# Kernel optimization log

Measured on AMD Instinct MI355X. Metric: run time of the kernel, lower is better.

The kernel has to match this reference:

```python
import jax, jax.numpy as jnp
import numpy as np

N_EMBED = 2048
N_HEAD = 16
HEAD_SIZE = N_EMBED // N_HEAD  # 128


def rotate_half(x):
    x1, x2 = jnp.split(x, 2, axis=-1)
    return jnp.concatenate((-x2, x1), axis=-1)


def setup_inputs() -> dict:
    key = jax.random.key(0)
    k_x, k_qkv, k_proj, k_b = jax.random.split(key, 4)
    B, T = 4, 2048
    x = jax.random.normal(k_x, (B, T, N_EMBED), dtype=jnp.float32)
    # weights stored as [in, out] so y = x @ W (equivalent param'n of nn.Linear)
    w_qkv = jax.random.normal(k_qkv, (N_EMBED, 3 * N_EMBED), dtype=jnp.float32) * (N_EMBED ** -0.5)
    w_proj = jax.random.normal(k_proj, (N_EMBED, N_EMBED), dtype=jnp.float32) * (N_EMBED ** -0.5)
    b_proj = jax.random.normal(k_b, (N_EMBED,), dtype=jnp.float32) * 0.02
    return {"x": x, "w_qkv": w_qkv, "w_proj": w_proj, "b_proj": b_proj}


def reference(x, w_qkv, w_proj, b_proj):
    B, T, C = x.shape
    H, D = N_HEAD, HEAD_SIZE
    qkv = x @ w_qkv                                   # [B,T,3C]
    q, k, v = jnp.split(qkv, 3, axis=2)
    q = q.reshape(B, T, H, D).transpose(0, 2, 1, 3)   # [B,H,T,D]
    k = k.reshape(B, T, H, D).transpose(0, 2, 1, 3)
    v = v.reshape(B, T, H, D).transpose(0, 2, 1, 3)
    # RoPE in fp32
    inv_freq = 1.0 / (10000.0 ** (jnp.arange(0, D, 2, dtype=jnp.float32) / D))
    t = jnp.arange(T, dtype=jnp.float32)
    freqs = jnp.einsum('i,j->ij', t, inv_freq)        # [T,D/2]
    emb = jnp.concatenate((freqs, freqs), axis=-1)    # [T,D]
    cos = jnp.cos(emb)[None, None, :, :]
    sin = jnp.sin(emb)[None, None, :, :]
    qf = q.astype(jnp.float32)
    kf = k.astype(jnp.float32)
    q = (qf * cos + rotate_half(qf) * sin).astype(v.dtype)
    k = (kf * cos + rotate_half(kf) * sin).astype(v.dtype)
    # causal SDPA
    scale = 1.0 / jnp.sqrt(jnp.asarray(D, dtype=q.dtype))
    scores = jnp.einsum('bhqd,bhkd->bhqk', q, k) * scale
    causal = jnp.tril(jnp.ones((T, T), dtype=bool))
    scores = jnp.where(causal[None, None, :, :], scores, jnp.finfo(scores.dtype).min)
    attn = jax.nn.softmax(scores, axis=-1)
    out = jnp.einsum('bhqk,bhkd->bhqd', attn, v)      # [B,H,T,D]
    out = out.transpose(0, 2, 1, 3).reshape(B, T, C)
    return out @ w_proj + b_proj
```

## Files before the change

kernel.cpp:

```cpp
#include <hip/hip_runtime.h>
#include <hip/hip_bf16.h>
#include <cstdint>
#include <cstddef>

typedef __bf16 bf16x8 __attribute__((ext_vector_type(8)));
typedef __bf16 bf16x4 __attribute__((ext_vector_type(4)));
typedef float  f32x4  __attribute__((ext_vector_type(4)));

__device__ __forceinline__ void lds_load16(const void* gsrc, void* ldst) {
    __builtin_amdgcn_global_load_lds(
        (const __attribute__((address_space(1))) unsigned int*)gsrc,
        (__attribute__((address_space(3))) unsigned int*)ldst,
        16, 0, 0);
}

__global__ __launch_bounds__(256) void cvt_k(const float* __restrict__ in,
                                             __bf16* __restrict__ out, int n8) {
    int i = blockIdx.x * 256 + threadIdx.x;
    if (i >= n8) return;
    const float4* p4 = (const float4*)in + (size_t)i * 2;
    float4 a = p4[0], b = p4[1];
    bf16x8 o;
    o[0] = (__bf16)a.x; o[1] = (__bf16)a.y; o[2] = (__bf16)a.z; o[3] = (__bf16)a.w;
    o[4] = (__bf16)b.x; o[5] = (__bf16)b.y; o[6] = (__bf16)b.z; o[7] = (__bf16)b.w;
    *((bf16x8*)out + i) = o;
}

__global__ __launch_bounds__(256) void transp_k(const float* __restrict__ W,
                                                __bf16* __restrict__ WT, int R, int C) {
    __shared__ float tile[32][33];
    int tx = threadIdx.x & 31, ty = threadIdx.x >> 5;
    int c0 = blockIdx.x * 32, r0 = blockIdx.y * 32;
#pragma unroll
    for (int k = 0; k < 4; ++k)
        tile[ty + 8 * k][tx] = W[(size_t)(r0 + ty + 8 * k) * C + c0 + tx];
    __syncthreads();
#pragma unroll
    for (int k = 0; k < 4; ++k)
        WT[(size_t)(c0 + ty + 8 * k) * R + r0 + tx] = (__bf16)tile[tx][ty + 8 * k];
}

__global__ __launch_bounds__(256) void sincos_k(float2* __restrict__ sc) {
    int idx = blockIdx.x * 256 + threadIdx.x;
    int t = idx >> 6, j = idx & 63;
    float inv = powf(10000.f, -(float)j / 64.f);
    float f = (float)t * inv;
    float s, c;
    sincosf(f, &s, &c);
    sc[idx] = make_float2(c, s);
}

__global__ __launch_bounds__(512, 2) void gemm8_k(const __bf16* __restrict__ A,
                                                  const __bf16* __restrict__ Bt,
                                                  int nbn, int mode,
                                                  __bf16* __restrict__ qb, __bf16* __restrict__ kb,
                                                  __bf16* __restrict__ vt,
                                                  float* __restrict__ outp,
                                                  const float* __restrict__ bias,
                                                  const float2* __restrict__ sc) {
    __shared__ __bf16 lds[2][2][2][128 * 64];
    const int K = 2048, NT = K / 64;
    int nwg = gridDim.x;
    int per = nwg >> 3;
    int bid = blockIdx.x;
    int wg = (bid & 7) * per + (bid >> 3);
    int bm = wg / nbn, bn = wg % nbn;
    int m0 = bm * 256, n0 = bn * 256;
    int tid = threadIdx.x;
    int lane = tid & 63, wave = tid >> 6;
    int wm = wave >> 2, wn = wave & 3;
    int lr = lane & 15, lg = lane >> 4;

    f32x4 acc[8][4] = {};

    auto stageA = [&](int db, int sub, int kt) {
#pragma unroll
        for (int l = 0; l < 2; ++l) {
            int chunk = l * 512 + tid;
            int r = chunk >> 3, c16 = chunk & 7;
            int rg = m0 + ((r >> 6) << 7) + (sub << 6) + (r & 63);
            lds_load16(A + (size_t)rg * K + (kt << 6) + ((c16 ^ (r & 7)) << 3),
                       &lds[db][0][sub][chunk * 8]);
        }
    };
    auto stageB = [&](int db, int sub, int kt) {
#pragma unroll
        for (int l = 0; l < 2; ++l) {
            int chunk = l * 512 + tid;
            int r = chunk >> 3, c16 = chunk & 7;
            int rg = n0 + ((r >> 5) << 6) + (sub << 5) + (r & 31);
            lds_load16(Bt + (size_t)rg * K + (kt << 6) + ((c16 ^ (r & 7)) << 3),
                       &lds[db][1][sub][chunk * 8]);
        }
    };
    auto rdA = [&](int db, int sub, int q, int kk) -> bf16x8 {
        int r = (wm << 6) + (q << 4) + lr;
        int cb = ((kk << 6) + (lg << 4)) ^ ((r & 7) << 4);
        return *(const bf16x8*)((const char*)&lds[db][0][sub][0] + r * 128 + cb);
    };
    auto rdB = [&](int db, int j, int kk) -> bf16x8 {
        int sub = j >> 1;
        int r = (wn << 5) + ((j & 1) << 4) + lr;
        int cb = ((kk << 6) + (lg << 4)) ^ ((r & 7) << 4);
        return *(const bf16x8*)((const char*)&lds[db][1][sub][0] + r * 128 + cb);
    };

    stageA(0, 0, 0); stageB(0, 0, 0); stageB(0, 1, 0); stageA(0, 1, 0);
    stageA(1, 0, 1); stageB(1, 0, 1);
    asm volatile("s_waitcnt vmcnt(8)" ::: "memory");
    __builtin_amdgcn_s_barrier();

    bf16x8 a[4][2], bA[2][2], bB[2][2];
    for (int t = 0; t < NT; ++t) {
        int db = t & 1, dn = db ^ 1;
        bool pf1 = (t + 1 < NT), pf2 = (t + 2 < NT);
#pragma unroll
        for (int q = 0; q < 4; ++q) { a[q][0] = rdA(db, 0, q, 0); a[q][1] = rdA(db, 0, q, 1); }
#pragma unroll
        for (int j = 0; j < 2; ++j) { bA[j][0] = rdB(db, j, 0); bA[j][1] = rdB(db, j, 1); }
        if (pf1) stageB(dn, 1, t + 1);
        __builtin_amdgcn_s_barrier();
        asm volatile("s_waitcnt lgkmcnt(0)" ::: "memory");
        __builtin_amdgcn_sched_barrier(0);
        __builtin_amdgcn_s_setprio(1);
#pragma unroll
        for (int q = 0; q < 4; ++q)
#pragma unroll
            for (int j = 0; j < 2; ++j)
#pragma unroll
                for (int kk = 0; kk < 2; ++kk)
                    acc[q][j] = __builtin_amdgcn_mfma_f32_16x16x32_bf16(a[q][kk], bA[j][kk], acc[q][j], 0, 0, 0);
        __builtin_amdgcn_s_setprio(0);
        if (pf2) asm volatile("s_waitcnt vmcnt(6)" ::: "memory");
        else     asm volatile("s_waitcnt vmcnt(0)" ::: "memory");
        __builtin_amdgcn_s_barrier();
#pragma unroll
        for (int j = 0; j < 2; ++j) { bB[j][0] = rdB(db, j + 2, 0); bB[j][1] = rdB(db, j + 2, 1); }
        if (pf1) stageA(dn, 1, t + 1);
        __builtin_amdgcn_s_barrier();
        asm volatile("s_waitcnt lgkmcnt(0)" ::: "memory");
        __builtin_amdgcn_sched_barrier(0);
        __builtin_amdgcn_s_setprio(1);
#pragma unroll
        for (int q = 0; q < 4; ++q)
#pragma unroll
            for (int j = 0; j < 2; ++j)
#pragma unroll
                for (int kk = 0; kk < 2; ++kk)
                    acc[q][j + 2] = __builtin_amdgcn_mfma_f32_16x16x32_bf16(a[q][kk], bB[j][kk], acc[q][j + 2], 0, 0, 0);
        __builtin_amdgcn_s_setprio(0);
        __builtin_amdgcn_s_barrier();
#pragma unroll
        for (int q = 0; q < 4; ++q) { a[q][0] = rdA(db, 1, q, 0); a[q][1] = rdA(db, 1, q, 1); }
        if (pf2) stageA(db, 0, t + 2);
        __builtin_amdgcn_s_barrier();
        asm volatile("s_waitcnt lgkmcnt(0)" ::: "memory");
        __builtin_amdgcn_sched_barrier(0);
        __builtin_amdgcn_s_setprio(1);
#pragma unroll
        for (int q = 0; q < 4; ++q)
#pragma unroll
            for (int j = 0; j < 2; ++j)
#pragma unroll
                for (int kk = 0; kk < 2; ++kk)
                    acc[q + 4][j + 2] = __builtin_amdgcn_mfma_f32_16x16x32_bf16(a[q][kk], bB[j][kk], acc[q + 4][j + 2], 0, 0, 0);
        __builtin_amdgcn_s_setprio(0);
        __builtin_amdgcn_s_barrier();
        if (pf2) stageB(db, 0, t + 2);
        __builtin_amdgcn_s_setprio(1);
#pragma unroll
        for (int q = 0; q < 4; ++q)
#pragma unroll
            for (int j = 0; j < 2; ++j)
#pragma unroll
                for (int kk = 0; kk < 2; ++kk)
                    acc[q + 4][j] = __builtin_amdgcn_mfma_f32_16x16x32_bf16(a[q][kk], bA[j][kk], acc[q + 4][j], 0, 0, 0);
        __builtin_amdgcn_s_setprio(0);
        if (pf2)      asm volatile("s_waitcnt vmcnt(8)" ::: "memory");
        else if (pf1) asm volatile("s_waitcnt vmcnt(4)" ::: "memory");
        __builtin_amdgcn_s_barrier();
    }

    if (mode == 0) {
        int which = n0 >> 11;
        if (which == 2) {
#pragma unroll
            for (int q = 0; q < 8; ++q) {
                int row_t = (wm << 7) + ((q >> 2) << 6) + ((q & 3) << 4) + (lg << 2);
#pragma unroll
                for (int j = 0; j < 4; ++j) {
                    int c = n0 + (wn << 6) + (j << 4) + lr;
                    int h = (c & 2047) >> 7, d = c & 127;
#pragma unroll
                    for (int r = 0; r < 4; ++r) {
                        int row = m0 + row_t + r;
                        int b_ = row >> 11, tt = row & 2047;
                        vt[((size_t)(b_ * 16 + h) * 128 + d) * 2048 + tt] = (__bf16)acc[q][j][r];
                    }
                }
            }
        } else {
            __bf16* dst = (which == 0) ? qb : kb;
            float scale = (which == 0) ? 0.08838834764831845f : 1.f;
            int rl = (wm << 4) + (lg << 2);
            int colw = (wn << 6);
#pragma unroll
            for (int q = 0; q < 8; ++q) {
                float* scr = (float*)&lds[q & 1][0][0][0];
                int row_t = (wm << 7) + ((q >> 2) << 6) + ((q & 3) << 4) + (lg << 2);
#pragma unroll
                for (int j = 0; j < 4; ++j)
#pragma unroll
                    for (int r = 0; r < 4; ++r)
                        scr[(rl + r) * 260 + colw + (j << 4) + lr] = acc[q][j][r];
                __syncthreads();
#pragma unroll
                for (int j = 0; j < 4; ++j) {
                    int c = n0 + colw + (j << 4) + lr;
                    int h = (c & 2047) >> 7, d = c & 127;
                    int jj = (j << 4) + lr;
#pragma unroll
                    for (int r = 0; r < 4; ++r) {
                        int row = m0 + row_t + r;
                        int b_ = row >> 11, tt = row & 2047;
                        float2 cs = sc[tt * 64 + jj];
                        float v0 = acc[q][j][r];
                        float v1 = scr[(rl + r) * 260 + (colw ^ 64) + (j << 4) + lr];
                        float o = ((wn & 1) == 0) ? (v0 * cs.x - v1 * cs.y)
                                                  : (v0 * cs.x + v1 * cs.y);
                        dst[((size_t)(b_ * 16 + h) * 2048 + tt) * 128 + d] = (__bf16)(o * scale);
                    }
                }
            }
        }
    } else {
#pragma unroll
        for (int q = 0; q < 8; ++q) {
            int row_t = (wm << 7) + ((q >> 2) << 6) + ((q & 3) << 4) + (lg << 2);
#pragma unroll
            for (int j = 0; j < 4; ++j) {
                int col = n0 + (wn << 6) + (j << 4) + lr;
                float bv = bias[col];
#pragma unroll
                for (int r = 0; r < 4; ++r) {
                    int row = m0 + row_t + r;
                    outp[(size_t)row * 2048 + col] = acc[q][j][r] + bv;
                }
            }
        }
    }
}

__global__ __launch_bounds__(512, 2) void attn_k(const __bf16* __restrict__ qb,
                                                 const __bf16* __restrict__ kb,
                                                 const __bf16* __restrict__ vt,
                                                 __bf16* __restrict__ ao) {
    __shared__ __bf16 Ks[64 * 128];
    __shared__ __bf16 Vs[128 * 64];
    __shared__ __bf16 Ps[8][16 * 64];

    int bid = blockIdx.x;
    int qt = 15 - (bid >> 6);
    int bh = bid & 63;
    int qs = qt * 128;
    int tid = threadIdx.x, wave = tid >> 6, lane = tid & 63;
    int lr = lane & 15, lg = lane >> 4;

    bf16x8 qf[4];
    const __bf16* Qrow = qb + ((size_t)bh * 2048 + qs + wave * 16 + lr) * 128;
#pragma unroll
    for (int kk = 0; kk < 4; ++kk) qf[kk] = *(const bf16x8*)(Qrow + kk * 32 + lg * 8);

    f32x4 ot[8] = {};
    float m_run = -1e30f, l_run = 0.f;
    int qmax = qs + wave * 16 + 15;
    int kend = qs + 64;

    for (int ks = 0; ks <= kend; ks += 64) {
#pragma unroll
        for (int i = 0; i < 2; ++i) {
            int c = tid + i * 512;
            {
                int row = c >> 4;
                int cc = c ^ (row & 7);
                int dd = (cc & 15) * 8;
                lds_load16(kb + ((size_t)bh * 2048 + ks + row) * 128 + dd, Ks + c * 8);
            }
            {
                int row = c >> 3;
                int cc = c ^ (row & 7);
                int tt = (cc & 7) * 8;
                lds_load16(vt + ((size_t)bh * 128 + row) * 2048 + ks + tt, Vs + c * 8);
            }
        }
        __syncthreads();

        if (ks <= qmax) {
            f32x4 st[4];
            __builtin_amdgcn_s_setprio(1);
#pragma unroll
            for (int mt = 0; mt < 4; ++mt) {
                f32x4 s = {};
#pragma unroll
                for (int kk = 0; kk < 4; ++kk) {
                    int row = mt * 16 + lr;
                    const __bf16* kp = Ks + row * 128 + ((((kk * 64 + lg * 16)) ^ ((row & 7) << 4)) >> 1);
                    bf16x8 afr = *(const bf16x8*)kp;
                    s = __builtin_amdgcn_mfma_f32_16x16x32_bf16(afr, qf[kk], s, 0, 0, 0);
                }
                st[mt] = s;
            }
            __builtin_amdgcn_s_setprio(0);

            if (ks + 63 > qs + wave * 16) {
                int q = qs + wave * 16 + lr;
#pragma unroll
                for (int mt = 0; mt < 4; ++mt)
#pragma unroll
                    for (int r = 0; r < 4; ++r) {
                        int kv = ks + mt * 16 + lg * 4 + r;
                        if (kv > q) st[mt][r] = -1e30f;
                    }
            }

            float pm = -1e30f;
#pragma unroll
            for (int mt = 0; mt < 4; ++mt)
#pragma unroll
                for (int r = 0; r < 4; ++r) pm = fmaxf(pm, st[mt][r]);
            pm = fmaxf(pm, __shfl_xor(pm, 16));
            pm = fmaxf(pm, __shfl_xor(pm, 32));
            float nm = fmaxf(m_run, pm);
            float alpha = __expf(m_run - nm);
            float psum = 0.f;
#pragma unroll
            for (int mt = 0; mt < 4; ++mt)
#pragma unroll
                for (int r = 0; r < 4; ++r) {
                    float p = __expf(st[mt][r] - nm);
                    psum += p;
                    st[mt][r] = p;
                }
            psum += __shfl_xor(psum, 16);
            psum += __shfl_xor(psum, 32);
            l_run = l_run * alpha + psum;
            m_run = nm;
#pragma unroll
            for (int t8 = 0; t8 < 8; ++t8) ot[t8] *= alpha;

#pragma unroll
            for (int mt = 0; mt < 4; ++mt) {
                bf16x4 pk;
#pragma unroll
                for (int r = 0; r < 4; ++r) pk[r] = (__bf16)st[mt][r];
                int byteoff = lr * 128 + (((mt * 32 + lg * 8)) ^ ((lr & 7) << 4));
                *(bf16x4*)((char*)&Ps[wave][0] + byteoff) = pk;
            }

            bf16x8 pfr[2];
#pragma unroll
            for (int kk = 0; kk < 2; ++kk) {
                const char* pp = (const char*)&Ps[wave][0] + lr * 128 + (((kk * 64 + lg * 16)) ^ ((lr & 7) << 4));
                pfr[kk] = *(const bf16x8*)pp;
            }
            __builtin_amdgcn_s_setprio(1);
#pragma unroll
            for (int dt = 0; dt < 8; ++dt) {
#pragma unroll
                for (int kk = 0; kk < 2; ++kk) {
                    int row = dt * 16 + lr;
                    const __bf16* vp = Vs + row * 64 + ((((kk * 64 + lg * 16)) ^ ((row & 7) << 4)) >> 1);
                    bf16x8 afr = *(const bf16x8*)vp;
                    ot[dt] = __builtin_amdgcn_mfma_f32_16x16x32_bf16(afr, pfr[kk], ot[dt], 0, 0, 0);
                }
            }
            __builtin_amdgcn_s_setprio(0);
        }
        __syncthreads();
    }

    float inv = 1.f / l_run;
    int b_ = bh >> 4, h = bh & 15;
    size_t rowbase = ((size_t)b_ * 2048 + qs + wave * 16 + lr) * 2048 + h * 128;
#pragma unroll
    for (int dt = 0; dt < 8; ++dt) {
        bf16x4 o;
#pragma unroll
        for (int r = 0; r < 4; ++r) o[r] = (__bf16)(ot[dt][r] * inv);
        *(bf16x4*)(ao + rowbase + dt * 16 + lg * 4) = o;
    }
}

extern "C" void kernel_launch(void* const* d_in, const int* in_sizes, int n_in,
                              void* d_out, int out_size, void* d_ws, size_t ws_size,
                              hipStream_t stream) {
    const float* x      = (const float*)d_in[0];
    const float* w_qkv  = (const float*)d_in[1];
    const float* w_proj = (const float*)d_in[2];
    const float* b_proj = (const float*)d_in[3];
    float* out = (float*)d_out;
    char* ws = (char*)d_ws;

    __bf16* xb  = (__bf16*)(ws);
    __bf16* wqt = (__bf16*)(ws + 33554432);
    __bf16* wpt = (__bf16*)(ws + 58720256);
    __bf16* qb  = (__bf16*)(ws + 67108864);
    __bf16* kb  = (__bf16*)(ws + 100663296);
    __bf16* vt  = (__bf16*)(ws + 134217728);
    __bf16* ao  = (__bf16*)(ws + 167772160);
    float2* sc  = (float2*)(ws + 201326592);

    hipLaunchKernelGGL(cvt_k, dim3(8192), dim3(256), 0, stream, x, xb, 2097152);
    hipLaunchKernelGGL(transp_k, dim3(192, 64), dim3(256), 0, stream, w_qkv, wqt, 2048, 6144);
    hipLaunchKernelGGL(transp_k, dim3(64, 64), dim3(256), 0, stream, w_proj, wpt, 2048, 2048);
    hipLaunchKernelGGL(sincos_k, dim3(512), dim3(256), 0, stream, sc);
    hipLaunchKernelGGL(gemm8_k, dim3(768), dim3(512), 0, stream,
                       xb, wqt, 24, 0, qb, kb, vt, (float*)nullptr, (const float*)nullptr, sc);
    hipLaunchKernelGGL(attn_k, dim3(1024), dim3(512), 0, stream, qb, kb, vt, ao);
    hipLaunchKernelGGL(gemm8_k, dim3(256), dim3(512), 0, stream,
                       ao, wpt, 8, 1, (__bf16*)nullptr, (__bf16*)nullptr, (__bf16*)nullptr,
                       out, b_proj, (const float2*)nullptr);
}
```

Before: 394.8 us.

## Merge prep kernels into one launch and add lazy softmax rescaling

The four preprocessing kernels (x conversion, two weight transposes, sincos table) become a single launch whose blocks branch on block index, cutting launch overhead and inter-kernel gaps. Separately, the attention online softmax now skips the max update and output rescaling whenever the new tile max stays within 8 of the running max across the wavefront. That avoids one exp and the eight output multiplies per tile, at the cost of a wave-uniform vote. Because exponent arguments can then reach e^8, there is a small overflow and precision risk in bf16 P.

```diff
diff --git a/kernel.cpp b/kernel.cpp
--- a/kernel.cpp
+++ b/kernel.cpp
@@ -14,40 +14,51 @@
         16, 0, 0);
 }
 
-__global__ __launch_bounds__(256) void cvt_k(const float* __restrict__ in,
-                                             __bf16* __restrict__ out, int n8) {
-    int i = blockIdx.x * 256 + threadIdx.x;
-    if (i >= n8) return;
-    const float4* p4 = (const float4*)in + (size_t)i * 2;
-    float4 a = p4[0], b = p4[1];
-    bf16x8 o;
-    o[0] = (__bf16)a.x; o[1] = (__bf16)a.y; o[2] = (__bf16)a.z; o[3] = (__bf16)a.w;
-    o[4] = (__bf16)b.x; o[5] = (__bf16)b.y; o[6] = (__bf16)b.z; o[7] = (__bf16)b.w;
-    *((bf16x8*)out + i) = o;
-}
-
-__global__ __launch_bounds__(256) void transp_k(const float* __restrict__ W,
-                                                __bf16* __restrict__ WT, int R, int C) {
+__global__ __launch_bounds__(256) void prep_k(const float* __restrict__ x,
+                                              __bf16* __restrict__ xb,
+                                              const float* __restrict__ w_qkv,
+                                              __bf16* __restrict__ wqt,
+                                              const float* __restrict__ w_proj,
+                                              __bf16* __restrict__ wpt,
+                                              float2* __restrict__ sc) {
     __shared__ float tile[32][33];
-    int tx = threadIdx.x & 31, ty = threadIdx.x >> 5;
-    int c0 = blockIdx.x * 32, r0 = blockIdx.y * 32;
-#pragma unroll
-    for (int k = 0; k < 4; ++k)
-        tile[ty + 8 * k][tx] = W[(size_t)(r0 + ty + 8 * k) * C + c0 + tx];
-    __syncthreads();
-#pragma unroll
-    for (int k = 0; k < 4; ++k)
-        WT[(size_t)(c0 + ty + 8 * k) * R + r0 + tx] = (__bf16)tile[tx][ty + 8 * k];
-}
-
-__global__ __launch_bounds__(256) void sincos_k(float2* __restrict__ sc) {
-    int idx = blockIdx.x * 256 + threadIdx.x;
-    int t = idx >> 6, j = idx & 63;
-    float inv = powf(10000.f, -(float)j / 64.f);
-    float f = (float)t * inv;
-    float s, c;
-    sincosf(f, &s, &c);
-    sc[idx] = make_float2(c, s);
+    int bid = blockIdx.x;
+    int tid = threadIdx.x;
+    if (bid < 8192) {
+        int i = bid * 256 + tid;
+        const float4* p4 = (const float4*)x + (size_t)i * 2;
+        float4 a = p4[0], b = p4[1];
+        bf16x8 o;
+        o[0] = (__bf16)a.x; o[1] = (__bf16)a.y; o[2] = (__bf16)a.z; o[3] = (__bf16)a.w;
+        o[4] = (__bf16)b.x; o[5] = (__bf16)b.y; o[6] = (__bf16)b.z; o[7] = (__bf16)b.w;
+        *((bf16x8*)xb + i) = o;
+    } else if (bid < 24576) {
+        const float* W; __bf16* WT; int R, C, bx, by;
+        if (bid < 20480) {
+            int b = bid - 8192; bx = b % 192; by = b / 192;
+            W = w_qkv; WT = wqt; R = 2048; C = 6144;
+        } else {
+            int b = bid - 20480; bx = b & 63; by = b >> 6;
+            W = w_proj; WT = wpt; R = 2048; C = 2048;
+        }
+        int tx = tid & 31, ty = tid >> 5;
+        int c0 = bx * 32, r0 = by * 32;
+#pragma unroll
+        for (int k = 0; k < 4; ++k)
+            tile[ty + 8 * k][tx] = W[(size_t)(r0 + ty + 8 * k) * C + c0 + tx];
+        __syncthreads();
+#pragma unroll
+        for (int k = 0; k < 4; ++k)
+            WT[(size_t)(c0 + ty + 8 * k) * R + r0 + tx] = (__bf16)tile[tx][ty + 8 * k];
+    } else {
+        int idx = (bid - 24576) * 256 + tid;
+        int t = idx >> 6, j = idx & 63;
+        float inv = powf(10000.f, -(float)j / 64.f);
+        float f = (float)t * inv;
+        float s, c;
+        sincosf(f, &s, &c);
+        sc[idx] = make_float2(c, s);
+    }
 }
 
 __global__ __launch_bounds__(512, 2) void gemm8_k(const __bf16* __restrict__ A,
@@ -330,23 +341,38 @@
                 for (int r = 0; r < 4; ++r) pm = fmaxf(pm, st[mt][r]);
             pm = fmaxf(pm, __shfl_xor(pm, 16));
             pm = fmaxf(pm, __shfl_xor(pm, 32));
-            float nm = fmaxf(m_run, pm);
-            float alpha = __expf(m_run - nm);
+
             float psum = 0.f;
-#pragma unroll
-            for (int mt = 0; mt < 4; ++mt)
-#pragma unroll
-                for (int r = 0; r < 4; ++r) {
-                    float p = __expf(st[mt][r] - nm);
-                    psum += p;
-                    st[mt][r] = p;
-                }
-            psum += __shfl_xor(psum, 16);
-            psum += __shfl_xor(psum, 32);
-            l_run = l_run * alpha + psum;
-            m_run = nm;
-#pragma unroll
-            for (int t8 = 0; t8 < 8; ++t8) ot[t8] *= alpha;
+            if (__all(pm <= m_run + 8.f)) {
+#pragma unroll
+                for (int mt = 0; mt < 4; ++mt)
+#pragma unroll
+                    for (int r = 0; r < 4; ++r) {
+                        float p = __expf(st[mt][r] - m_run);
+                        psum += p;
+                        st[mt][r] = p;
+                    }
+                psum += __shfl_xor(psum, 16);
+                psum += __shfl_xor(psum, 32);
+                l_run += psum;
+            } else {
+                float nm = fmaxf(m_run, pm);
+                float alpha = __expf(m_run - nm);
+#pragma unroll
+                for (int mt = 0; mt < 4; ++mt)
+#pragma unroll
+                    for (int r = 0; r < 4; ++r) {
+                        float p = __expf(st[mt][r] - nm);
+                        psum += p;
+                        st[mt][r] = p;
+                    }
+                psum += __shfl_xor(psum, 16);
+                psum += __shfl_xor(psum, 32);
+                l_run = l_run * alpha + psum;
+                m_run = nm;
+#pragma unroll
+                for (int t8 = 0; t8 < 8; ++t8) ot[t8] *= alpha;
+            }
 
 #pragma unroll
             for (int mt = 0; mt < 4; ++mt) {
@@ -410,10 +436,8 @@
     __bf16* ao  = (__bf16*)(ws + 167772160);
     float2* sc  = (float2*)(ws + 201326592);
 
-    hipLaunchKernelGGL(cvt_k, dim3(8192), dim3(256), 0, stream, x, xb, 2097152);
-    hipLaunchKernelGGL(transp_k, dim3(192, 64), dim3(256), 0, stream, w_qkv, wqt, 2048, 6144);
-    hipLaunchKernelGGL(transp_k, dim3(64, 64), dim3(256), 0, stream, w_proj, wpt, 2048, 2048);
-    hipLaunchKernelGGL(sincos_k, dim3(512), dim3(256), 0, stream, sc);
+    hipLaunchKernelGGL(prep_k, dim3(25088), dim3(256), 0, stream,
+                       x, xb, w_qkv, wqt, w_proj, wpt, sc);
     hipLaunchKernelGGL(gemm8_k, dim3(768), dim3(512), 0, stream,
                        xb, wqt, 24, 0, qb, kb, vt, (float*)nullptr, (const float*)nullptr, sc);
     hipLaunchKernelGGL(attn_k, dim3(1024), dim3(512), 0, stream, qb, kb, vt, ao);
```

Measured after the change: 433.7 us. 1.1x slower.
